# Optimization experiments

Hardware: AMD Instinct MI355X
Metric: run time of the kernel (lower is better)

## Reference

```python
import jax, jax.numpy as jnp
import numpy as np

D_HEAD = 64
NOISE_STD = 0.01


def setup_inputs() -> dict:
    key = jax.random.key(0)
    ks = jax.random.split(key, 5)
    B, T, D, H, Dh = 2, 2048, 1024, 16, D_HEAD
    std = 0.02 * Dh ** 0.5
    return {
        "residual_stream": jax.random.normal(ks[0], (B, T, D), jnp.float32),
        "W_Q": jax.random.normal(ks[1], (H, D, Dh), jnp.float32) * std,
        "W_K": jax.random.normal(ks[2], (H, D, Dh), jnp.float32) * std,
        "W_V": jax.random.normal(ks[3], (H, D, Dh), jnp.float32) * std,
        "W_output": jax.random.normal(ks[4], (H, Dh, D), jnp.float32) * std,
        "b_Q": jnp.zeros((H, Dh), jnp.float32),
        "b_K": jnp.zeros((H, Dh), jnp.float32),
        "b_V": jnp.zeros((H, Dh), jnp.float32),
        "b_output": jnp.zeros((D,), jnp.float32),
    }


def reference(residual_stream, W_Q, W_K, W_V, W_output, b_Q, b_K, b_V, b_output):
    B, T, D = residual_stream.shape
    H = W_Q.shape[0]
    # per-head QKV projections: [B,T,H,Dh]
    q = jnp.einsum("btd,hde->bthe", residual_stream, W_Q) + b_Q
    k = jnp.einsum("btd,hde->bthe", residual_stream, W_K) + b_K
    v = jnp.einsum("btd,hde->bthe", residual_stream, W_V) + b_V
    # scaled scores [B,H,Tq,Tk]
    scores = jnp.einsum("bqhe,bkhe->bhqk", q, k) / (D_HEAD ** 0.5)
    # causal mask (upper triangle, diagonal=1 excluded)
    causal = jnp.tril(jnp.ones((T, T), dtype=bool))
    scores = jnp.where(causal, scores, -jnp.inf)
    # noise injected after masking (-inf + noise stays -inf)
    noise = jax.random.normal(jax.random.key(42), scores.shape, scores.dtype) * NOISE_STD
    pattern = jax.nn.softmax(scores + noise, axis=-1)
    z = jnp.einsum("bkhe,bhqk->bqhe", v, pattern)
    out = jnp.einsum("bthe,hed->btd", z, W_output) + b_output
    return out
```

## Files before the change

kernel.cpp:

```cpp
#include <hip/hip_runtime.h>

#define BB 2
#define HH 16
#define TT 2048
#define DD 1024
#define DH 64

typedef _Float16 half8 __attribute__((ext_vector_type(8)));
typedef _Float16 half4v __attribute__((ext_vector_type(4)));
typedef float f32x4 __attribute__((ext_vector_type(4)));

#define GLOAD(g, l)                                                        \
    __builtin_amdgcn_global_load_lds(                                      \
        (const __attribute__((address_space(1))) unsigned int*)(g),        \
        (__attribute__((address_space(3))) unsigned int*)(l), 16, 0, 0)

__global__ __launch_bounds__(256) void cvt_all_kernel(
    const float* __restrict__ x,
    const float* __restrict__ Wq, const float* __restrict__ Wk,
    const float* __restrict__ Wv, const float* __restrict__ Wo,
    _Float16* __restrict__ xh, _Float16* __restrict__ Wt,
    _Float16* __restrict__ Wot)
{
    const int bid = blockIdx.x;
    const int tid = threadIdx.x;
    __shared__ float ts[64][68];

    if (bid < 2048) {
        size_t i = ((size_t)bid * 256 + tid) * 8;
        float4 a = *(const float4*)&x[i];
        float4 b = *(const float4*)&x[i + 4];
        half8 o;
        o[0] = (_Float16)a.x; o[1] = (_Float16)a.y; o[2] = (_Float16)a.z; o[3] = (_Float16)a.w;
        o[4] = (_Float16)b.x; o[5] = (_Float16)b.y; o[6] = (_Float16)b.z; o[7] = (_Float16)b.w;
        *(half8*)&xh[i] = o;
        return;
    }

    if (bid < 2816) {
        const int r = bid - 2048;
        const int d0 = (r & 15) * 64;
        const int h = (r >> 4) & 15;
        const int m = r >> 8;
        const float* __restrict__ W = (m == 0) ? Wq : (m == 1) ? Wk : Wv;

        const int dr = tid >> 2, ec = (tid & 3) * 16;
        const float* p = W + ((size_t)h * DD + d0 + dr) * DH + ec;
        *(float4*)&ts[dr][ec + 0]  = *(const float4*)(p + 0);
        *(float4*)&ts[dr][ec + 4]  = *(const float4*)(p + 4);
        *(float4*)&ts[dr][ec + 8]  = *(const float4*)(p + 8);
        *(float4*)&ts[dr][ec + 12] = *(const float4*)(p + 12);
        __syncthreads();

        const int er = tid >> 2, dc = (tid & 3) * 16;
        size_t obase = ((size_t)m * 1024 + h * 64 + er) * 1024 + d0 + dc;
        half8 o;
#pragma unroll
        for (int j = 0; j < 8; ++j) o[j] = (_Float16)ts[dc + j][er];
        *(half8*)&Wt[obase] = o;
#pragma unroll
        for (int j = 0; j < 8; ++j) o[j] = (_Float16)ts[dc + 8 + j][er];
        *(half8*)&Wt[obase + 8] = o;
        return;
    }

    {
        const int r = bid - 2816;
        const int r0 = (r & 15) * 64;
        const int c0 = (r >> 4) * 64;

        const int rr = tid >> 2, cc = (tid & 3) * 16;
        const float* p = Wo + (size_t)(r0 + rr) * 1024 + c0 + cc;
        *(float4*)&ts[rr][cc + 0]  = *(const float4*)(p + 0);
        *(float4*)&ts[rr][cc + 4]  = *(const float4*)(p + 4);
        *(float4*)&ts[rr][cc + 8]  = *(const float4*)(p + 8);
        *(float4*)&ts[rr][cc + 12] = *(const float4*)(p + 12);
        __syncthreads();

        const int er = tid >> 2, dc = (tid & 3) * 16;
        size_t obase = (size_t)(c0 + er) * 1024 + r0 + dc;
        half8 o;
#pragma unroll
        for (int j = 0; j < 8; ++j) o[j] = (_Float16)ts[dc + j][er];
        *(half8*)&Wot[obase] = o;
#pragma unroll
        for (int j = 0; j < 8; ++j) o[j] = (_Float16)ts[dc + 8 + j][er];
        *(half8*)&Wot[obase + 8] = o;
    }
}

#define GEMM_MAIN(Aptr, Bptr, lda, ldb, KDIM)                                   \
    __shared__ _Float16 As[128 * 64];                                           \
    __shared__ _Float16 Bs[128 * 64];                                           \
    const int tid = threadIdx.x;                                                \
    const int wave = tid >> 6, lane = tid & 63;                                 \
    const int quad = lane >> 4, l15 = lane & 15;                                \
    const int rowBase = blockIdx.x * 128;                                       \
    const int colBase = blockIdx.y * 128;                                       \
    const int wr = (wave >> 1) * 64, wc = (wave & 1) * 64;                      \
    f32x4 acc[4][4];                                                            \
    _Pragma("unroll") for (int sm = 0; sm < 4; ++sm)                            \
        _Pragma("unroll") for (int sn = 0; sn < 4; ++sn)                        \
            acc[sm][sn] = f32x4{0.f, 0.f, 0.f, 0.f};                            \
    for (int k0 = 0; k0 < (KDIM); k0 += 64) {                                   \
        __syncthreads();                                                        \
        _Pragma("unroll") for (int i = 0; i < 4; ++i) {                         \
            int c = wave * 256 + i * 64 + lane;                                 \
            int row = c >> 3, c8 = c & 7;                                       \
            int sc = ((c8 ^ (row & 7)) << 3);                                   \
            GLOAD((Aptr) + (size_t)(rowBase + row) * (lda) + k0 + sc,           \
                  &As[(wave * 256 + i * 64) * 8]);                              \
            GLOAD((Bptr) + (size_t)(colBase + row) * (ldb) + k0 + sc,           \
                  &Bs[(wave * 256 + i * 64) * 8]);                              \
        }                                                                       \
        __syncthreads();                                                        \
        _Pragma("unroll") for (int kk = 0; kk < 2; ++kk) {                      \
            half8 af[4], bf[4];                                                 \
            _Pragma("unroll") for (int s = 0; s < 4; ++s) {                     \
                int rm = wr + s * 16 + l15;                                     \
                af[s] = *(const half8*)&As[rm * 64 +                            \
                        (((kk * 4 + quad) ^ (rm & 7)) << 3)];                   \
                int rn = wc + s * 16 + l15;                                     \
                bf[s] = *(const half8*)&Bs[rn * 64 +                            \
                        (((kk * 4 + quad) ^ (rn & 7)) << 3)];                   \
            }                                                                   \
            _Pragma("unroll") for (int sm = 0; sm < 4; ++sm)                    \
                _Pragma("unroll") for (int sn = 0; sn < 4; ++sn)                \
                    acc[sm][sn] = __builtin_amdgcn_mfma_f32_16x16x32_f16(       \
                        af[sm], bf[sn], acc[sm][sn], 0, 0, 0);                  \
        }                                                                       \
    }

__global__ __launch_bounds__(256) void qkv_gemm_kernel(
    const _Float16* __restrict__ xh, const _Float16* __restrict__ Wt,
    const float* __restrict__ bq, const float* __restrict__ bk, const float* __restrict__ bv,
    _Float16* __restrict__ qh, _Float16* __restrict__ kh, _Float16* __restrict__ vt)
{
    GEMM_MAIN(xh, Wt, 1024, 1024, 1024)

    const int m = colBase >> 10;
    const int nIn = colBase & 1023;
    const float* __restrict__ bias = (m == 0) ? bq : (m == 1) ? bk : bv;
    const float sc_ = (m == 0) ? 0.18033688f : 1.0f;

    if (m < 2) {
        _Float16* __restrict__ out = (m == 0) ? qh : kh;
#pragma unroll
        for (int sn = 0; sn < 4; ++sn) {
            int n = nIn + wc + sn * 16 + l15;
            int hh = n >> 6, e = n & 63;
            float bv_ = bias[n];
#pragma unroll
            for (int sm = 0; sm < 4; ++sm)
#pragma unroll
                for (int reg = 0; reg < 4; ++reg) {
                    int t = rowBase + wr + sm * 16 + quad * 4 + reg;
                    int bb = t >> 11, tt = t & (TT - 1);
                    out[(((size_t)bb * HH + hh) * TT + tt) * DH + e] =
                        (_Float16)((acc[sm][sn][reg] + bv_) * sc_);
                }
        }
    } else {
#pragma unroll
        for (int sn = 0; sn < 4; ++sn) {
            int n = nIn + wc + sn * 16 + l15;
            int hh = n >> 6, e = n & 63;
            float bv_ = bias[n];
#pragma unroll
            for (int sm = 0; sm < 4; ++sm) {
                int t = rowBase + wr + sm * 16 + quad * 4;
                int bb = t >> 11, tt = t & (TT - 1);
                int tile = tt >> 6, tp = tt & 63;
                half4v o;
#pragma unroll
                for (int reg = 0; reg < 4; ++reg)
                    o[reg] = (_Float16)(acc[sm][sn][reg] + bv_);
                *(half4v*)&vt[(((size_t)bb * HH + hh) * 32 + tile) * 4096 +
                              (size_t)e * 64 + tp] = o;
            }
        }
    }
}

__global__ __launch_bounds__(256) void out_gemm_kernel(
    const _Float16* __restrict__ zh, const _Float16* __restrict__ Wot,
    const float* __restrict__ bo, float* __restrict__ out)
{
    __shared__ _Float16 As[64 * 64];
    __shared__ _Float16 Bs[128 * 64];
    const int tid = threadIdx.x;
    const int wave = tid >> 6, lane = tid & 63;
    const int quad = lane >> 4, l15 = lane & 15;
    const int rowBase = blockIdx.x * 64;
    const int colBase = blockIdx.y * 128;
    const int wr = (wave >> 1) * 32, wc = (wave & 1) * 64;

    f32x4 acc[2][4];
#pragma unroll
    for (int sm = 0; sm < 2; ++sm)
#pragma unroll
        for (int sn = 0; sn < 4; ++sn) acc[sm][sn] = f32x4{0.f, 0.f, 0.f, 0.f};

    for (int k0 = 0; k0 < 1024; k0 += 64) {
        __syncthreads();
#pragma unroll
        for (int i = 0; i < 2; ++i) {
            int c = i * 256 + tid;
            int row = c >> 3, c8 = c & 7;
            GLOAD(zh + (size_t)(rowBase + row) * 1024 + k0 + ((c8 ^ (row & 7)) << 3),
                  &As[(i * 256 + wave * 64) * 8]);
        }
#pragma unroll
        for (int i = 0; i < 4; ++i) {
            int c = i * 256 + tid;
            int row = c >> 3, c8 = c & 7;
            GLOAD(Wot + (size_t)(colBase + row) * 1024 + k0 + ((c8 ^ (row & 7)) << 3),
                  &Bs[(i * 256 + wave * 64) * 8]);
        }
        __syncthreads();
#pragma unroll
        for (int kk = 0; kk < 2; ++kk) {
            half8 af[2], bf[4];
#pragma unroll
            for (int s = 0; s < 2; ++s) {
                int rm = wr + s * 16 + l15;
                af[s] = *(const half8*)&As[rm * 64 + (((kk * 4 + quad) ^ (rm & 7)) << 3)];
            }
#pragma unroll
            for (int s = 0; s < 4; ++s) {
                int rn = wc + s * 16 + l15;
                bf[s] = *(const half8*)&Bs[rn * 64 + (((kk * 4 + quad) ^ (rn & 7)) << 3)];
            }
#pragma unroll
            for (int sm = 0; sm < 2; ++sm)
#pragma unroll
                for (int sn = 0; sn < 4; ++sn)
                    acc[sm][sn] = __builtin_amdgcn_mfma_f32_16x16x32_f16(
                        af[sm], bf[sn], acc[sm][sn], 0, 0, 0);
        }
    }

#pragma unroll
    for (int sn = 0; sn < 4; ++sn) {
        int d = colBase + wc + sn * 16 + l15;
        float b_ = bo[d];
#pragma unroll
        for (int sm = 0; sm < 2; ++sm)
#pragma unroll
            for (int reg = 0; reg < 4; ++reg) {
                int r = rowBase + wr + sm * 16 + quad * 4 + reg;
                out[(size_t)r * 1024 + d] = acc[sm][sn][reg] + b_;
            }
    }
}

#define ATTN_LDS (8192 + 8192 + 16384 + 16384)

__global__ __launch_bounds__(256) void attn_kernel(
    const _Float16* __restrict__ qh, const _Float16* __restrict__ kh,
    const _Float16* __restrict__ vt, _Float16* __restrict__ zh)
{
    __shared__ __align__(16) char smem[ATTN_LDS];
    _Float16* qsA = (_Float16*)smem;
    _Float16* qsB = (_Float16*)(smem + 8192);
    _Float16* ks  = (_Float16*)(smem + 16384);
    _Float16* vs  = (_Float16*)(smem + 32768);
    _Float16* ps  = qsB;

    const int tid  = threadIdx.x;
    const int wave = tid >> 6;
    const int lane = tid & 63;
    const int quad = lane >> 4;
    const int l15  = lane & 15;
    const int p = blockIdx.x;
    const int h = blockIdx.y;
    const int b = blockIdx.z;
    const int qA = 31 - p;
    const int qB = p;

    const size_t headBase = ((size_t)b * HH + h) * (size_t)(TT * DH);
    const _Float16* qpA = qh + headBase + (size_t)qA * 64 * 64;
    const _Float16* qpB = qh + headBase + (size_t)qB * 64 * 64;
    const _Float16* kp  = kh + headBase;
    const _Float16* vtp = vt + ((size_t)b * HH + h) * 32 * 4096;

    half8 ones;
#pragma unroll
    for (int i = 0; i < 8; ++i) ones[i] = (_Float16)1.0f;

    auto stage_kv = [&](int s) {
        const int par = s & 1;
#pragma unroll
        for (int it = 0; it < 2; ++it) {
            int c = it * 256 + tid;
            int row = c >> 3, c8 = c & 7;
            size_t off = (size_t)s * 4096 + row * 64 + ((c8 ^ (row & 7)) << 3);
            GLOAD(kp + off,  &ks[par * 4096 + (it * 256 + wave * 64) * 8]);
            GLOAD(vtp + off, &vs[par * 4096 + (it * 256 + wave * 64) * 8]);
        }
    };

#pragma unroll
    for (int it = 0; it < 2; ++it) {
        int c = it * 256 + tid;
        int row = c >> 3, c8 = c & 7;
        size_t o = (size_t)row * 64 + ((c8 ^ (row & 7)) << 3);
        GLOAD(qpA + o, &qsA[(it * 256 + wave * 64) * 8]);
        GLOAD(qpB + o, &qsB[(it * 256 + wave * 64) * 8]);
    }
    stage_kv(0);
    __syncthreads();

    const int rmq = wave * 16 + l15;
    const int swq = rmq & 7;
    half8 aq[2][2];
    aq[0][0] = *(const half8*)&qsA[rmq * 64 + ((quad ^ swq) << 3)];
    aq[0][1] = *(const half8*)&qsA[rmq * 64 + (((4 + quad) ^ swq) << 3)];
    aq[1][0] = *(const half8*)&qsB[rmq * 64 + ((quad ^ swq) << 3)];
    aq[1][1] = *(const half8*)&qsB[rmq * 64 + (((4 + quad) ^ swq) << 3)];

    f32x4 accO[2][4];
    float mrow[2][4], lsum[2][4];
#pragma unroll
    for (int t = 0; t < 2; ++t)
#pragma unroll
        for (int j = 0; j < 4; ++j) {
            accO[t][j] = f32x4{0.f, 0.f, 0.f, 0.f};
            mrow[t][j] = -1e30f;
            lsum[t][j] = 0.f;
        }

    auto compute_tile = [&](int t, const _Float16* curK, const _Float16* curV,
                            bool diag) {
        f32x4 S[4];
#pragma unroll
        for (int j = 0; j < 4; ++j) {
            if (diag && j > wave) {
                S[j] = f32x4{-1e30f, -1e30f, -1e30f, -1e30f};
                continue;
            }
            int rn = j * 16 + l15, sw = rn & 7;
            half8 b0 = *(const half8*)&curK[rn * 64 + ((quad ^ sw) << 3)];
            half8 b1 = *(const half8*)&curK[rn * 64 + (((4 + quad) ^ sw) << 3)];
            f32x4 a = f32x4{0.f, 0.f, 0.f, 0.f};
            a = __builtin_amdgcn_mfma_f32_16x16x32_f16(aq[t][0], b0, a, 0, 0, 0);
            a = __builtin_amdgcn_mfma_f32_16x16x32_f16(aq[t][1], b1, a, 0, 0, 0);
            S[j] = a;
        }

        if (diag) {
#pragma unroll
            for (int jj = 0; jj < 4; ++jj) {
                if (jj != wave) continue;
                int col = jj * 16 + l15;
#pragma unroll
                for (int reg = 0; reg < 4; ++reg)
                    if (col > wave * 16 + quad * 4 + reg) S[jj][reg] = -1e30f;
            }
        }

#pragma unroll
        for (int reg = 0; reg < 4; ++reg) {
            float mt = fmaxf(fmaxf(S[0][reg], S[1][reg]),
                             fmaxf(S[2][reg], S[3][reg]));
            mt = fmaxf(mt, __shfl_xor(mt, 1));
            mt = fmaxf(mt, __shfl_xor(mt, 2));
            mt = fmaxf(mt, __shfl_xor(mt, 4));
            mt = fmaxf(mt, __shfl_xor(mt, 8));
            float mnew = fmaxf(mrow[t][reg], mt);
            float alpha = exp2f(mrow[t][reg] - mnew);
            mrow[t][reg] = mnew;
            lsum[t][reg] *= alpha;
#pragma unroll
            for (int j = 0; j < 4; ++j) {
                S[j][reg] = exp2f(S[j][reg] - mnew);
                accO[t][j][reg] *= alpha;
            }
        }

        const int prow = wave * 16 + quad * 4;
#pragma unroll
        for (int j = 0; j < 4; ++j)
#pragma unroll
            for (int reg = 0; reg < 4; ++reg) {
                int c = j * 16 + l15;
                int r = prow + reg;
                ps[r * 64 + (((c >> 3) ^ (r & 7)) << 3) + (c & 7)] =
                    (_Float16)S[j][reg];
            }

        half8 ap0 = *(const half8*)&ps[rmq * 64 + ((quad ^ swq) << 3)];
        half8 ap1 = *(const half8*)&ps[rmq * 64 + (((4 + quad) ^ swq) << 3)];

        {
            f32x4 psum = f32x4{0.f, 0.f, 0.f, 0.f};
            psum = __builtin_amdgcn_mfma_f32_16x16x32_f16(ap0, ones, psum, 0, 0, 0);
            psum = __builtin_amdgcn_mfma_f32_16x16x32_f16(ap1, ones, psum, 0, 0, 0);
#pragma unroll
            for (int reg = 0; reg < 4; ++reg) lsum[t][reg] += psum[reg];
        }

#pragma unroll
        for (int j = 0; j < 4; ++j) {
            int rn = j * 16 + l15, sw = rn & 7;
            half8 bv0 = *(const half8*)&curV[rn * 64 + ((quad ^ sw) << 3)];
            half8 bv1 = *(const half8*)&curV[rn * 64 + (((4 + quad) ^ sw) << 3)];
            accO[t][j] = __builtin_amdgcn_mfma_f32_16x16x32_f16(ap0, bv0, accO[t][j], 0, 0, 0);
            accO[t][j] = __builtin_amdgcn_mfma_f32_16x16x32_f16(ap1, bv1, accO[t][j], 0, 0, 0);
        }
    };

    for (int s = 0; s <= qA; ++s) {
        if (s < qA) stage_kv(s + 1);

        const _Float16* curK = &ks[(s & 1) * 4096];
        const _Float16* curV = &vs[(s & 1) * 4096];

        compute_tile(0, curK, curV, s == qA);
        if (s <= qB) compute_tile(1, curK, curV, s == qB);

        __syncthreads();
    }

#pragma unroll
    for (int t = 0; t < 2; ++t) {
        const int Q0 = (t == 0 ? qA : qB) * 64;
#pragma unroll
        for (int reg = 0; reg < 4; ++reg) {
            float inv = 1.f / lsum[t][reg];
            int tt = Q0 + wave * 16 + quad * 4 + reg;
            size_t rowOff = ((size_t)b * TT + tt) * DD + h * DH;
#pragma unroll
            for (int j = 0; j < 4; ++j)
                zh[rowOff + j * 16 + l15] = (_Float16)(accO[t][j][reg] * inv);
        }
    }
}

extern "C" void kernel_launch(void* const* d_in, const int* in_sizes, int n_in,
                              void* d_out, int out_size, void* d_ws, size_t ws_size,
                              hipStream_t stream) {
    const float* x  = (const float*)d_in[0];
    const float* Wq = (const float*)d_in[1];
    const float* Wk = (const float*)d_in[2];
    const float* Wv = (const float*)d_in[3];
    const float* Wo = (const float*)d_in[4];
    const float* bq = (const float*)d_in[5];
    const float* bk = (const float*)d_in[6];
    const float* bv = (const float*)d_in[7];
    const float* bo = (const float*)d_in[8];
    float* out = (float*)d_out;

    const size_t MB = 1u << 20;
    char* wsb = (char*)d_ws;
    _Float16* xh  = (_Float16*)(wsb + 0 * MB);
    _Float16* Wt  = (_Float16*)(wsb + 8 * MB);
    _Float16* Wot = (_Float16*)(wsb + 14 * MB);
    _Float16* qh  = (_Float16*)(wsb + 16 * MB);
    _Float16* kh  = (_Float16*)(wsb + 24 * MB);
    _Float16* vt  = (_Float16*)(wsb + 32 * MB);
    _Float16* zh  = (_Float16*)(wsb + 40 * MB);

    cvt_all_kernel<<<3072, 256, 0, stream>>>(x, Wq, Wk, Wv, Wo, xh, Wt, Wot);
    qkv_gemm_kernel<<<dim3(32, 24), 256, 0, stream>>>(xh, Wt, bq, bk, bv, qh, kh, vt);
    attn_kernel<<<dim3(16, HH, BB), 256, 0, stream>>>(qh, kh, vt, zh);
    out_gemm_kernel<<<dim3(64, 8), 256, 0, stream>>>(zh, Wot, bo, out);
}
```

Measured before the change: 222.5 us.

## Share K/V fragment loads across both query tiles and swizzle GEMM block order

The attention loop now loads the K and V fragments from shared memory once per KV step and reuses them for both query tiles. Before, each tile reloaded them inside its own compute call. Both QK score sets are computed before the softmax so the MFMAs can interleave. Separately, the QKV and output GEMMs remap the linear block index so groups of four consecutive blocks share a row tile, which is meant to improve L2 reuse. Holding the K/V fragments and both score sets in registers at once raises register pressure and could reduce occupancy.

Result: no change. 218.7 us (-1.7%).

```diff
diff --git a/kernel.cpp b/kernel.cpp
--- a/kernel.cpp
+++ b/kernel.cpp
@@ -89,14 +89,14 @@
     }
 }
 
-#define GEMM_MAIN(Aptr, Bptr, lda, ldb, KDIM)                                   \
+#define GEMM_MAIN(Aptr, Bptr, lda, ldb, KDIM, BX, BY)                           \
     __shared__ _Float16 As[128 * 64];                                           \
     __shared__ _Float16 Bs[128 * 64];                                           \
     const int tid = threadIdx.x;                                                \
     const int wave = tid >> 6, lane = tid & 63;                                 \
     const int quad = lane >> 4, l15 = lane & 15;                                \
-    const int rowBase = blockIdx.x * 128;                                       \
-    const int colBase = blockIdx.y * 128;                                       \
+    const int rowBase = (BX) * 128;                                             \
+    const int colBase = (BY) * 128;                                             \
     const int wr = (wave >> 1) * 64, wc = (wave & 1) * 64;                      \
     f32x4 acc[4][4];                                                            \
     _Pragma("unroll") for (int sm = 0; sm < 4; ++sm)                            \
@@ -136,7 +136,10 @@
     const float* __restrict__ bq, const float* __restrict__ bk, const float* __restrict__ bv,
     _Float16* __restrict__ qh, _Float16* __restrict__ kh, _Float16* __restrict__ vt)
 {
-    GEMM_MAIN(xh, Wt, 1024, 1024, 1024)
+    const int lin = blockIdx.y * 32 + blockIdx.x;
+    const int bx_ = (lin >> 2) & 31;
+    const int by_ = (lin & 3) + 4 * (lin >> 7);
+    GEMM_MAIN(xh, Wt, 1024, 1024, 1024, bx_, by_)
 
     const int m = colBase >> 10;
     const int nIn = colBase & 1023;
@@ -191,8 +194,9 @@
     const int tid = threadIdx.x;
     const int wave = tid >> 6, lane = tid & 63;
     const int quad = lane >> 4, l15 = lane & 15;
-    const int rowBase = blockIdx.x * 64;
-    const int colBase = blockIdx.y * 128;
+    const int lin = blockIdx.y * 64 + blockIdx.x;
+    const int rowBase = ((lin >> 2) & 63) * 64;
+    const int colBase = ((lin & 3) + 4 * (lin >> 8)) * 128;
     const int wr = (wave >> 1) * 32, wc = (wave & 1) * 64;
 
     f32x4 acc[2][4];
@@ -330,35 +334,7 @@
             lsum[t][j] = 0.f;
         }
 
-    auto compute_tile = [&](int t, const _Float16* curK, const _Float16* curV,
-                            bool diag) {
-        f32x4 S[4];
-#pragma unroll
-        for (int j = 0; j < 4; ++j) {
-            if (diag && j > wave) {
-                S[j] = f32x4{-1e30f, -1e30f, -1e30f, -1e30f};
-                continue;
-            }
-            int rn = j * 16 + l15, sw = rn & 7;
-            half8 b0 = *(const half8*)&curK[rn * 64 + ((quad ^ sw) << 3)];
-            half8 b1 = *(const half8*)&curK[rn * 64 + (((4 + quad) ^ sw) << 3)];
-            f32x4 a = f32x4{0.f, 0.f, 0.f, 0.f};
-            a = __builtin_amdgcn_mfma_f32_16x16x32_f16(aq[t][0], b0, a, 0, 0, 0);
-            a = __builtin_amdgcn_mfma_f32_16x16x32_f16(aq[t][1], b1, a, 0, 0, 0);
-            S[j] = a;
-        }
-
-        if (diag) {
-#pragma unroll
-            for (int jj = 0; jj < 4; ++jj) {
-                if (jj != wave) continue;
-                int col = jj * 16 + l15;
-#pragma unroll
-                for (int reg = 0; reg < 4; ++reg)
-                    if (col > wave * 16 + quad * 4 + reg) S[jj][reg] = -1e30f;
-            }
-        }
-
+    auto finish_tile = [&](int t, f32x4* S, const half8* bv0, const half8* bv1) {
 #pragma unroll
         for (int reg = 0; reg < 4; ++reg) {
             float mt = fmaxf(fmaxf(S[0][reg], S[1][reg]),
@@ -402,11 +378,8 @@
 
 #pragma unroll
         for (int j = 0; j < 4; ++j) {
-            int rn = j * 16 + l15, sw = rn & 7;
-            half8 bv0 = *(const half8*)&curV[rn * 64 + ((quad ^ sw) << 3)];
-            half8 bv1 = *(const half8*)&curV[rn * 64 + (((4 + quad) ^ sw) << 3)];
-            accO[t][j] = __builtin_amdgcn_mfma_f32_16x16x32_f16(ap0, bv0, accO[t][j], 0, 0, 0);
-            accO[t][j] = __builtin_amdgcn_mfma_f32_16x16x32_f16(ap1, bv1, accO[t][j], 0, 0, 0);
+            accO[t][j] = __builtin_amdgcn_mfma_f32_16x16x32_f16(ap0, bv0[j], accO[t][j], 0, 0, 0);
+            accO[t][j] = __builtin_amdgcn_mfma_f32_16x16x32_f16(ap1, bv1[j], accO[t][j], 0, 0, 0);
         }
     };
 
@@ -415,9 +388,75 @@
 
         const _Float16* curK = &ks[(s & 1) * 4096];
         const _Float16* curV = &vs[(s & 1) * 4096];
-
-        compute_tile(0, curK, curV, s == qA);
-        if (s <= qB) compute_tile(1, curK, curV, s == qB);
+        const bool bAct  = (s <= qB);
+        const bool diagA = (s == qA);
+        const bool diagB = (s == qB);
+
+        half8 bk0[4], bk1[4];
+#pragma unroll
+        for (int j = 0; j < 4; ++j) {
+            int rn = j * 16 + l15, sw = rn & 7;
+            bk0[j] = *(const half8*)&curK[rn * 64 + ((quad ^ sw) << 3)];
+            bk1[j] = *(const half8*)&curK[rn * 64 + (((4 + quad) ^ sw) << 3)];
+        }
+
+        f32x4 SA[4], SB[4];
+#pragma unroll
+        for (int j = 0; j < 4; ++j) {
+            if (diagA && j > wave) {
+                SA[j] = f32x4{-1e30f, -1e30f, -1e30f, -1e30f};
+            } else {
+                f32x4 a = f32x4{0.f, 0.f, 0.f, 0.f};
+                a = __builtin_amdgcn_mfma_f32_16x16x32_f16(aq[0][0], bk0[j], a, 0, 0, 0);
+                a = __builtin_amdgcn_mfma_f32_16x16x32_f16(aq[0][1], bk1[j], a, 0, 0, 0);
+                SA[j] = a;
+            }
+        }
+        if (bAct) {
+#pragma unroll
+            for (int j = 0; j < 4; ++j) {
+                if (diagB && j > wave) {
+                    SB[j] = f32x4{-1e30f, -1e30f, -1e30f, -1e30f};
+                } else {
+                    f32x4 a = f32x4{0.f, 0.f, 0.f, 0.f};
+                    a = __builtin_amdgcn_mfma_f32_16x16x32_f16(aq[1][0], bk0[j], a, 0, 0, 0);
+                    a = __builtin_amdgcn_mfma_f32_16x16x32_f16(aq[1][1], bk1[j], a, 0, 0, 0);
+                    SB[j] = a;
+                }
+            }
+        }
+
+        if (diagA) {
+#pragma unroll
+            for (int jj = 0; jj < 4; ++jj) {
+                if (jj != wave) continue;
+                int col = jj * 16 + l15;
+#pragma unroll
+                for (int reg = 0; reg < 4; ++reg)
+                    if (col > wave * 16 + quad * 4 + reg) SA[jj][reg] = -1e30f;
+            }
+        }
+        if (bAct && diagB) {
+#pragma unroll
+            for (int jj = 0; jj < 4; ++jj) {
+                if (jj != wave) continue;
+                int col = jj * 16 + l15;
+#pragma unroll
+                for (int reg = 0; reg < 4; ++reg)
+                    if (col > wave * 16 + quad * 4 + reg) SB[jj][reg] = -1e30f;
+            }
+        }
+
+        half8 bv0[4], bv1[4];
+#pragma unroll
+        for (int j = 0; j < 4; ++j) {
+            int rn = j * 16 + l15, sw = rn & 7;
+            bv0[j] = *(const half8*)&curV[rn * 64 + ((quad ^ sw) << 3)];
+            bv1[j] = *(const half8*)&curV[rn * 64 + (((4 + quad) ^ sw) << 3)];
+        }
+
+        finish_tile(0, SA, bv0, bv1);
+        if (bAct) finish_tile(1, SB, bv0, bv1);
 
         __syncthreads();
     }
```
